# Kernel tuning notes

Hardware: AMD Instinct MI355X
Metric: run time of the kernel (lower is better)

The kernel has to match this reference:

```python
import jax, jax.numpy as jnp
import numpy as np

EMBED_DIM = 256
UNITS = 512


def setup_inputs() -> dict:
    key = jax.random.key(0)
    k1, k2, k3, k4, k5, k6, k7, k8 = jax.random.split(key, 8)
    B, L = 2048, 64
    features = jax.random.normal(k1, (B, L, EMBED_DIM), dtype=jnp.float32)
    hidden = jax.random.normal(k2, (B, UNITS), dtype=jnp.float32)
    s1 = 1.0 / np.sqrt(EMBED_DIM)
    s2 = 1.0 / np.sqrt(UNITS)
    W1 = jax.random.normal(k3, (EMBED_DIM, UNITS), dtype=jnp.float32) * s1
    b1 = jnp.zeros((UNITS,), dtype=jnp.float32)
    W2 = jax.random.normal(k4, (UNITS, UNITS), dtype=jnp.float32) * s2
    b2 = jnp.zeros((UNITS,), dtype=jnp.float32)
    V = jax.random.normal(k5, (UNITS, 1), dtype=jnp.float32) * s2
    bV = jnp.zeros((1,), dtype=jnp.float32)
    return {"features": features, "hidden": hidden, "W1": W1, "b1": b1,
            "W2": W2, "b2": b2, "V": V, "bV": bV}


def reference(features, hidden, W1, b1, W2, b2, V, bV):
    # features: [B, L, D_feat]; hidden: [B, U]
    # score = tanh(W1(features) + W2(hidden)[:, None])  -> [B, L, U]
    proj_f = jnp.einsum('bld,du->blu', features, W1) + b1
    proj_h = hidden @ W2 + b2                         # [B, U]
    score = jnp.tanh(proj_f + proj_h[:, None, :])     # [B, L, U]
    logits = jnp.einsum('blu,uo->blo', score, V) + bV  # [B, L, 1]
    attention_weights = jax.nn.softmax(logits, axis=1)  # softmax over L
    context_vector = jnp.sum(attention_weights * features, axis=1)  # [B, D_feat]
    return context_vector, attention_weights
```

## Files before the change

### kernel.cpp

```cpp
#include <hip/hip_runtime.h>
#include <math.h>

#define B_N 2048
#define L_N 64
#define D_N 256
#define U_N 512

typedef __attribute__((ext_vector_type(8))) short bf16x8;
typedef __attribute__((ext_vector_type(4))) float f32x4;

__device__ __forceinline__ float fast_tanh(float x) {
    float e = __expf(2.0f * x);
    return 1.0f - 2.0f / (e + 1.0f);
}
__device__ __forceinline__ ushort f2bf(float x) {
    uint b = __float_as_uint(x);
    uint r = (b + 0x7FFF + ((b >> 16) & 1)) >> 16;
    return (ushort)r;
}
__device__ __forceinline__ float bf2f(ushort u) {
    uint v = ((uint)u) << 16;
    return __uint_as_float(v);
}

__global__ __launch_bounds__(256) void pack_w1(const float* __restrict__ W1,
                                               ushort* __restrict__ W1p) {
    int g = blockIdx.x * 256 + threadIdx.x;
    int ntg  = g >> 9;
    int ks   = (g >> 6) & 7;
    int lane = g & 63;
    int n  = ntg * 16 + (lane & 15);
    int kb = ks * 32 + (lane >> 4) * 8;
    ushort tmp[8];
#pragma unroll
    for (int j = 0; j < 8; ++j) tmp[j] = f2bf(W1[(kb + j) * U_N + n]);
    *(uint4*)&W1p[(size_t)g * 8] = *(uint4*)tmp;
}

__global__ __launch_bounds__(256) void proj_h_kernel(
    const float* __restrict__ hidden, const float* __restrict__ W2,
    const float* __restrict__ b1, const float* __restrict__ b2,
    ushort* __restrict__ ph)
{
    __shared__ float hs[8 * 512];
    __shared__ float w2s[64 * 128];

    const int t  = threadIdx.x;
    const int b0 = blockIdx.x * 8;
    const int u0 = blockIdx.y * 128;
    const int ug = t & 31;
    const int bg = t >> 5;

#pragma unroll
    for (int i = 0; i < 4; ++i) {
        int f4 = t + i * 256;
        *(float4*)&hs[(f4 >> 7) * 512 + (f4 & 127) * 4] =
            *(const float4*)&hidden[(b0 + (f4 >> 7)) * U_N + (f4 & 127) * 4];
    }

    float acc[4] = {0.f, 0.f, 0.f, 0.f};
    for (int kc = 0; kc < 8; ++kc) {
        __syncthreads();
#pragma unroll
        for (int i = 0; i < 8; ++i) {
            int f4 = t + i * 256;
            *(float4*)&w2s[(f4 >> 5) * 128 + (f4 & 31) * 4] =
                *(const float4*)&W2[(kc * 64 + (f4 >> 5)) * U_N + u0 + (f4 & 31) * 4];
        }
        __syncthreads();
        for (int k = 0; k < 64; k += 4) {
            float4 a4 = *(const float4*)&hs[bg * 512 + kc * 64 + k];
            const float* ap = (const float*)&a4;
#pragma unroll
            for (int kk = 0; kk < 4; ++kk) {
                float4 w4 = *(const float4*)&w2s[(k + kk) * 128 + ug * 4];
                float av = ap[kk];
                acc[0] = fmaf(av, w4.x, acc[0]);
                acc[1] = fmaf(av, w4.y, acc[1]);
                acc[2] = fmaf(av, w4.z, acc[2]);
                acc[3] = fmaf(av, w4.w, acc[3]);
            }
        }
    }

    const int u = u0 + ug * 4;
    float4 bb1 = *(const float4*)&b1[u];
    float4 bb2 = *(const float4*)&b2[u];
    ushort o[4] = {f2bf(acc[0] + bb1.x + bb2.x), f2bf(acc[1] + bb1.y + bb2.y),
                   f2bf(acc[2] + bb1.z + bb2.z), f2bf(acc[3] + bb1.w + bb2.w)};
    *(uint2*)&ph[(size_t)(b0 + bg) * U_N + u] = *(uint2*)o;
}

__global__ __launch_bounds__(256, 2) void attn_kernel(
    const float* __restrict__ features, const ushort* __restrict__ W1p,
    const float* __restrict__ V, const float* __restrict__ bV,
    const ushort* __restrict__ ph, float* __restrict__ out)
{
    __shared__ ushort As[64 * 256];
    __shared__ float lpart[4][64];
    __shared__ float wls[64];

    const int b    = blockIdx.x;
    const int t    = threadIdx.x;
    const int w    = t >> 6;
    const int lane = t & 63;
    const int ml   = lane & 15;
    const int q    = lane >> 4;
    const float* fb = features + (size_t)b * (L_N * D_N);

#pragma unroll
    for (int i = 0; i < 8; ++i) {
        int f = t + i * 256;
        int m = f >> 5, c = f & 31;
        float4 x0 = *(const float4*)&fb[m * D_N + c * 8];
        float4 x1 = *(const float4*)&fb[m * D_N + c * 8 + 4];
        ushort tmp[8] = {f2bf(x0.x), f2bf(x0.y), f2bf(x0.z), f2bf(x0.w),
                         f2bf(x1.x), f2bf(x1.y), f2bf(x1.z), f2bf(x1.w)};
        *(uint4*)&As[(m * 32 + (c ^ (m & 31))) * 8] = *(uint4*)tmp;
    }
    __syncthreads();

    f32x4 acc[4][8];
#pragma unroll
    for (int mt = 0; mt < 4; ++mt)
#pragma unroll
        for (int nt = 0; nt < 8; ++nt)
            acc[mt][nt] = (f32x4){0.f, 0.f, 0.f, 0.f};

    for (int ks = 0; ks < 8; ++ks) {
        bf16x8 a[4];
#pragma unroll
        for (int mt = 0; mt < 4; ++mt) {
            int m = mt * 16 + ml;
            int c = ks * 4 + q;
            a[mt] = *(const bf16x8*)&As[(m * 32 + (c ^ (m & 31))) * 8];
        }
        bf16x8 bf[8];
#pragma unroll
        for (int nt = 0; nt < 8; ++nt) {
            int chunk = ((w * 8 + nt) * 8 + ks) * 64 + lane;
            bf[nt] = *(const bf16x8*)&W1p[(size_t)chunk * 8];
        }
#pragma unroll
        for (int nt = 0; nt < 8; ++nt)
#pragma unroll
            for (int mt = 0; mt < 4; ++mt)
                acc[mt][nt] = __builtin_amdgcn_mfma_f32_16x16x32_bf16(
                    a[mt], bf[nt], acc[mt][nt], 0, 0, 0);
    }

    float lp[16];
#pragma unroll
    for (int j = 0; j < 16; ++j) lp[j] = 0.f;
#pragma unroll
    for (int nt = 0; nt < 8; ++nt) {
        int n = w * 128 + nt * 16 + ml;
        float phv = bf2f(ph[(size_t)b * U_N + n]);
        float vv  = V[n];
#pragma unroll
        for (int mt = 0; mt < 4; ++mt)
#pragma unroll
            for (int r = 0; r < 4; ++r) {
                float s = fast_tanh(acc[mt][nt][r] + phv);
                lp[mt * 4 + r] = fmaf(s, vv, lp[mt * 4 + r]);
            }
    }
#pragma unroll
    for (int off = 1; off <= 8; off <<= 1)
#pragma unroll
        for (int j = 0; j < 16; ++j)
            lp[j] += __shfl_xor(lp[j], off);
    if (ml == 0) {
#pragma unroll
        for (int mt = 0; mt < 4; ++mt)
#pragma unroll
            for (int r = 0; r < 4; ++r)
                lpart[w][mt * 16 + q * 4 + r] = lp[mt * 4 + r];
    }
    __syncthreads();

    if (t < 64) {
        float lsum = bV[0] + lpart[0][t] + lpart[1][t] + lpart[2][t] + lpart[3][t];
        float mx = lsum;
#pragma unroll
        for (int off = 32; off > 0; off >>= 1)
            mx = fmaxf(mx, __shfl_xor(mx, off));
        float e = __expf(lsum - mx);
        float ssum = e;
#pragma unroll
        for (int off = 32; off > 0; off >>= 1)
            ssum += __shfl_xor(ssum, off);
        float wt = e / ssum;
        wls[t] = wt;
        out[(size_t)B_N * D_N + (size_t)b * L_N + t] = wt;
    }
    __syncthreads();

    float ctx = 0.f;
#pragma unroll 16
    for (int l = 0; l < L_N; ++l) {
        ushort u = As[(l * 32 + ((t >> 3) ^ (l & 31))) * 8 + (t & 7)];
        ctx = fmaf(wls[l], bf2f(u), ctx);
    }
    out[(size_t)b * D_N + t] = ctx;
}

extern "C" void kernel_launch(void* const* d_in, const int* in_sizes, int n_in,
                              void* d_out, int out_size, void* d_ws, size_t ws_size,
                              hipStream_t stream) {
    const float* features = (const float*)d_in[0];
    const float* hidden   = (const float*)d_in[1];
    const float* W1       = (const float*)d_in[2];
    const float* b1       = (const float*)d_in[3];
    const float* W2       = (const float*)d_in[4];
    const float* b2       = (const float*)d_in[5];
    const float* V        = (const float*)d_in[6];
    const float* bV       = (const float*)d_in[7];
    float* out = (float*)d_out;

    ushort* ph  = (ushort*)d_ws;
    ushort* W1p = (ushort*)((char*)d_ws + (size_t)B_N * U_N * sizeof(ushort));

    pack_w1<<<64, 256, 0, stream>>>(W1, W1p);
    proj_h_kernel<<<dim3(B_N / 8, U_N / 128), 256, 0, stream>>>(hidden, W2, b1, b2, ph);
    attn_kernel<<<B_N, 256, 0, stream>>>(features, W1p, V, bV, ph, out);
}
```

Measured before the change: 307.4 us.

## Compute hidden projection with bf16 MFMA and pack W2 alongside W1

Replaces the FP32 scalar-FMA hidden@W2 kernel with a bf16 MFMA kernel that reads a pre-packed W2 layout. W2 packing is merged into the W1 packing kernel, so one launch handles both. The attention kernel's launch bounds are raised from 2 to 4 blocks per SM to push occupancy. In exchange, the hidden projection now runs in bf16, and the tighter register budget could cause spills in the 128-accumulator attention kernel.

```diff
diff --git a/kernel.cpp b/kernel.cpp
--- a/kernel.cpp
+++ b/kernel.cpp
@@ -23,75 +23,84 @@
     return __uint_as_float(v);
 }
 
-__global__ __launch_bounds__(256) void pack_w1(const float* __restrict__ W1,
-                                               ushort* __restrict__ W1p) {
-    int g = blockIdx.x * 256 + threadIdx.x;
-    int ntg  = g >> 9;
-    int ks   = (g >> 6) & 7;
-    int lane = g & 63;
-    int n  = ntg * 16 + (lane & 15);
-    int kb = ks * 32 + (lane >> 4) * 8;
+__global__ __launch_bounds__(256) void pack_weights(
+    const float* __restrict__ W1, const float* __restrict__ W2,
+    ushort* __restrict__ W1p, ushort* __restrict__ W2p)
+{
     ushort tmp[8];
-#pragma unroll
-    for (int j = 0; j < 8; ++j) tmp[j] = f2bf(W1[(kb + j) * U_N + n]);
-    *(uint4*)&W1p[(size_t)g * 8] = *(uint4*)tmp;
-}
-
-__global__ __launch_bounds__(256) void proj_h_kernel(
-    const float* __restrict__ hidden, const float* __restrict__ W2,
+    if (blockIdx.x < 64) {
+        int g = blockIdx.x * 256 + threadIdx.x;
+        int ntg = g >> 9, ks = (g >> 6) & 7, lane = g & 63;
+        int n  = ntg * 16 + (lane & 15);
+        int kb = ks * 32 + (lane >> 4) * 8;
+#pragma unroll
+        for (int j = 0; j < 8; ++j) tmp[j] = f2bf(W1[(kb + j) * U_N + n]);
+        *(uint4*)&W1p[(size_t)g * 8] = *(uint4*)tmp;
+    } else {
+        int g = (blockIdx.x - 64) * 256 + threadIdx.x;
+        int ntg = g >> 10, ks = (g >> 6) & 15, lane = g & 63;
+        int n  = ntg * 16 + (lane & 15);
+        int kb = ks * 32 + (lane >> 4) * 8;
+#pragma unroll
+        for (int j = 0; j < 8; ++j) tmp[j] = f2bf(W2[(kb + j) * U_N + n]);
+        *(uint4*)&W2p[(size_t)g * 8] = *(uint4*)tmp;
+    }
+}
+
+__global__ __launch_bounds__(256) void proj_h_mfma(
+    const float* __restrict__ hidden, const ushort* __restrict__ W2p,
     const float* __restrict__ b1, const float* __restrict__ b2,
     ushort* __restrict__ ph)
 {
-    __shared__ float hs[8 * 512];
-    __shared__ float w2s[64 * 128];
+    __shared__ ushort As[16 * 512];
 
     const int t  = threadIdx.x;
-    const int b0 = blockIdx.x * 8;
-    const int u0 = blockIdx.y * 128;
-    const int ug = t & 31;
-    const int bg = t >> 5;
+    const int b0 = blockIdx.x * 16;
+    const int u0 = blockIdx.y * 256;
 
 #pragma unroll
     for (int i = 0; i < 4; ++i) {
-        int f4 = t + i * 256;
-        *(float4*)&hs[(f4 >> 7) * 512 + (f4 & 127) * 4] =
-            *(const float4*)&hidden[(b0 + (f4 >> 7)) * U_N + (f4 & 127) * 4];
-    }
-
-    float acc[4] = {0.f, 0.f, 0.f, 0.f};
-    for (int kc = 0; kc < 8; ++kc) {
-        __syncthreads();
-#pragma unroll
-        for (int i = 0; i < 8; ++i) {
-            int f4 = t + i * 256;
-            *(float4*)&w2s[(f4 >> 5) * 128 + (f4 & 31) * 4] =
-                *(const float4*)&W2[(kc * 64 + (f4 >> 5)) * U_N + u0 + (f4 & 31) * 4];
+        int f = t + i * 256;
+        int m = f >> 6, c = f & 63;
+        float4 x0 = *(const float4*)&hidden[(b0 + m) * U_N + c * 8];
+        float4 x1 = *(const float4*)&hidden[(b0 + m) * U_N + c * 8 + 4];
+        ushort tmp[8] = {f2bf(x0.x), f2bf(x0.y), f2bf(x0.z), f2bf(x0.w),
+                         f2bf(x1.x), f2bf(x1.y), f2bf(x1.z), f2bf(x1.w)};
+        *(uint4*)&As[(m * 64 + c) * 8] = *(uint4*)tmp;
+    }
+    __syncthreads();
+
+    const int w = t >> 6, lane = t & 63;
+    const int ml = lane & 15, q = lane >> 4;
+
+    f32x4 acc[4];
+#pragma unroll
+    for (int nt = 0; nt < 4; ++nt) acc[nt] = (f32x4){0.f, 0.f, 0.f, 0.f};
+
+    for (int ks = 0; ks < 16; ++ks) {
+        bf16x8 a = *(const bf16x8*)&As[(ml * 64 + ks * 4 + q) * 8];
+        bf16x8 bb[4];
+#pragma unroll
+        for (int nt = 0; nt < 4; ++nt) {
+            int ntg = blockIdx.y * 16 + w * 4 + nt;
+            bb[nt] = *(const bf16x8*)&W2p[(size_t)((ntg * 16 + ks) * 64 + lane) * 8];
         }
-        __syncthreads();
-        for (int k = 0; k < 64; k += 4) {
-            float4 a4 = *(const float4*)&hs[bg * 512 + kc * 64 + k];
-            const float* ap = (const float*)&a4;
-#pragma unroll
-            for (int kk = 0; kk < 4; ++kk) {
-                float4 w4 = *(const float4*)&w2s[(k + kk) * 128 + ug * 4];
-                float av = ap[kk];
-                acc[0] = fmaf(av, w4.x, acc[0]);
-                acc[1] = fmaf(av, w4.y, acc[1]);
-                acc[2] = fmaf(av, w4.z, acc[2]);
-                acc[3] = fmaf(av, w4.w, acc[3]);
-            }
-        }
-    }
-
-    const int u = u0 + ug * 4;
-    float4 bb1 = *(const float4*)&b1[u];
-    float4 bb2 = *(const float4*)&b2[u];
-    ushort o[4] = {f2bf(acc[0] + bb1.x + bb2.x), f2bf(acc[1] + bb1.y + bb2.y),
-                   f2bf(acc[2] + bb1.z + bb2.z), f2bf(acc[3] + bb1.w + bb2.w)};
-    *(uint2*)&ph[(size_t)(b0 + bg) * U_N + u] = *(uint2*)o;
-}
-
-__global__ __launch_bounds__(256, 2) void attn_kernel(
+#pragma unroll
+        for (int nt = 0; nt < 4; ++nt)
+            acc[nt] = __builtin_amdgcn_mfma_f32_16x16x32_bf16(a, bb[nt], acc[nt], 0, 0, 0);
+    }
+
+#pragma unroll
+    for (int nt = 0; nt < 4; ++nt) {
+        int n = u0 + w * 64 + nt * 16 + ml;
+        float bias = b1[n] + b2[n];
+#pragma unroll
+        for (int r = 0; r < 4; ++r)
+            ph[(size_t)(b0 + q * 4 + r) * U_N + n] = f2bf(acc[nt][r] + bias);
+    }
+}
+
+__global__ __launch_bounds__(256, 4) void attn_kernel(
     const float* __restrict__ features, const ushort* __restrict__ W1p,
     const float* __restrict__ V, const float* __restrict__ bV,
     const ushort* __restrict__ ph, float* __restrict__ out)
@@ -219,9 +228,10 @@
     float* out = (float*)d_out;
 
     ushort* ph  = (ushort*)d_ws;
-    ushort* W1p = (ushort*)((char*)d_ws + (size_t)B_N * U_N * sizeof(ushort));
-
-    pack_w1<<<64, 256, 0, stream>>>(W1, W1p);
-    proj_h_kernel<<<dim3(B_N / 8, U_N / 128), 256, 0, stream>>>(hidden, W2, b1, b2, ph);
+    ushort* W1p = (ushort*)((char*)d_ws + (size_t)B_N * U_N * 2);
+    ushort* W2p = (ushort*)((char*)d_ws + (size_t)B_N * U_N * 2 + (size_t)D_N * U_N * 2);
+
+    pack_weights<<<192, 256, 0, stream>>>(W1, W2, W1p, W2p);
+    proj_h_mfma<<<dim3(B_N / 16, U_N / 256), 256, 0, stream>>>(hidden, W2p, b1, b2, ph);
     attn_kernel<<<B_N, 256, 0, stream>>>(features, W1p, V, bV, ph, out);
 }
```

After: 513.0 us. 1.67x slower.
